# Kernel tuning notes

Hardware: AMD Instinct MI355X
Metric: run time of the kernel (lower is better)

The kernel has to match this reference:

```python
import jax, jax.numpy as jnp
import numpy as np

N_NODES = 100000
N_EDGES = 1600000
IN_CH = 128
HID = 64


def gcn_conv(x, W, b, src, dst, n):
    """PyG-style GCNConv: add self-loops, symmetric deg^-1/2 normalization."""
    h = x @ W  # [n, out]
    # degree including self-loop, computed from destination (col) indices
    deg = jax.ops.segment_sum(jnp.ones_like(dst, dtype=h.dtype), dst, num_segments=n) + 1.0
    dinv = jax.lax.rsqrt(deg)  # [n]
    norm = dinv[src] * dinv[dst]  # [E]
    agg = jax.ops.segment_sum(h[src] * norm[:, None], dst, num_segments=n)
    agg = agg + h * (1.0 / deg)[:, None]  # self-loop term: norm = 1/deg
    return agg + b


def setup_inputs() -> dict:
    key = jax.random.key(0)
    ks = jax.random.split(key, 6)
    x = jax.random.normal(ks[0], (N_NODES, IN_CH), dtype=jnp.float32)
    edge_index = jax.random.randint(ks[1], (2, N_EDGES), 0, N_NODES, dtype=jnp.int64)
    W1 = jax.random.normal(ks[2], (IN_CH, HID), dtype=jnp.float32) / np.sqrt(IN_CH)
    b1 = jnp.zeros((HID,), dtype=jnp.float32)
    W2 = jax.random.normal(ks[3], (HID, HID), dtype=jnp.float32) / np.sqrt(HID)
    b2 = jnp.zeros((HID,), dtype=jnp.float32)
    Wl = jax.random.normal(ks[4], (HID, 1), dtype=jnp.float32) / np.sqrt(HID)
    bl = jnp.zeros((1,), dtype=jnp.float32)
    return {"x": x, "edge_index": edge_index, "W1": W1, "b1": b1,
            "W2": W2, "b2": b2, "Wl": Wl, "bl": bl}


def reference(x, edge_index, W1, b1, W2, b2, Wl, bl):
    src, dst = edge_index[0], edge_index[1]
    n = x.shape[0]
    h = gcn_conv(x, W1, b1, src, dst, n)
    h = jax.nn.relu(h)
    # dropout: identity in eval mode
    h = gcn_conv(h, W2, b2, src, dst, n)
    h = jax.nn.relu(h)
    out = (h @ Wl + bl)[:, 0]  # [n]
    return out
```

## Files before the change

### kernel.cpp

```cpp
#include <hip/hip_runtime.h>
#include <hip/hip_fp16.h>


#define SHIFT 9
#define BSZ   (1 << SHIFT)
#define NBMAX 256
#define BIN_CH 1024
#define PMAX  12288

using f16x8 = __attribute__((ext_vector_type(8))) _Float16;
using f16x2 = __attribute__((ext_vector_type(2))) _Float16;
using f32x4 = __attribute__((ext_vector_type(4))) float;

__global__ __launch_bounds__(256) void k_bin(const int* __restrict__ src,
                                             const int* __restrict__ dst,
                                             unsigned* __restrict__ binned,
                                             int* __restrict__ gbase,
                                             __half* __restrict__ hs,
                                             int n, int nb, int E) {
    if (blockIdx.x == 0 && threadIdx.x < 8) {
        uint4 z = {0u, 0u, 0u, 0u};
        reinterpret_cast<uint4*>(hs + ((size_t)n << 6))[threadIdx.x] = z;
    }
    __shared__ int h[NBMAX];
    __shared__ int ex[NBMAX + 1];
    __shared__ int cur[NBMAX];
    __shared__ int stmp[256];
    const int t = threadIdx.x;
    const int blk = blockIdx.x;
    const int beg = blk * BIN_CH;
    for (int i = t; i < NBMAX; i += 256) h[i] = 0;
    __syncthreads();
    const int e4 = beg + t * 4;
    const bool act = e4 < E;
    int4 d4 = {0, 0, 0, 0};
    if (act) {
        d4 = *reinterpret_cast<const int4*>(dst + e4);
        atomicAdd(&h[d4.x >> SHIFT], 1);
        atomicAdd(&h[d4.y >> SHIFT], 1);
        atomicAdd(&h[d4.z >> SHIFT], 1);
        atomicAdd(&h[d4.w >> SHIFT], 1);
    }
    __syncthreads();
    const int hv = (t < nb) ? h[t] : 0;
    stmp[t] = hv;
    __syncthreads();
    for (int off = 1; off < 256; off <<= 1) {
        int u = (t >= off) ? stmp[t - off] : 0;
        __syncthreads();
        stmp[t] += u;
        __syncthreads();
    }
    if (t <= nb) ex[t] = stmp[t] - ((t < nb) ? h[t] : 0);
    __syncthreads();
    if (t < nb) cur[t] = ex[t];
    if (t <= nb) gbase[(size_t)blk * (nb + 1) + t] = ex[t];
    __syncthreads();
    if (act) {
        const int4 s4 = *reinterpret_cast<const int4*>(src + e4);
        int b0 = d4.x >> SHIFT, b1 = d4.y >> SHIFT;
        int b2 = d4.z >> SHIFT, b3 = d4.w >> SHIFT;
        int p0 = atomicAdd(&cur[b0], 1);
        int p1 = atomicAdd(&cur[b1], 1);
        int p2 = atomicAdd(&cur[b2], 1);
        int p3 = atomicAdd(&cur[b3], 1);
        binned[beg + p0] = (unsigned)s4.x | ((unsigned)(d4.x & (BSZ - 1)) << 17);
        binned[beg + p1] = (unsigned)s4.y | ((unsigned)(d4.y & (BSZ - 1)) << 17);
        binned[beg + p2] = (unsigned)s4.z | ((unsigned)(d4.z & (BSZ - 1)) << 17);
        binned[beg + p3] = (unsigned)s4.w | ((unsigned)(d4.w & (BSZ - 1)) << 17);
    }
}

#define TD 32
__global__ __launch_bounds__(256) void k_xpose(const int* __restrict__ gbase,
                                               int* __restrict__ gbaseT,
                                               int nblk, int nbp1) {
    __shared__ int tile[TD][TD + 1];
    const int ctiles = (nbp1 + TD - 1) / TD;
    const int bx = blockIdx.x % ctiles;
    const int by = blockIdx.x / ctiles;
    const int c0 = bx * TD, r0 = by * TD;
    const int tx = threadIdx.x & 31, ty = threadIdx.x >> 5;
    for (int dy = ty; dy < TD; dy += 8) {
        int r = r0 + dy, c = c0 + tx;
        tile[dy][tx] = (r < nblk && c < nbp1) ? gbase[(size_t)r * nbp1 + c] : 0;
    }
    __syncthreads();
    for (int dy = ty; dy < TD; dy += 8) {
        int r = c0 + dy, c = r0 + tx;
        if (r < nbp1 && c < nblk)
            gbaseT[(size_t)r * nblk + c] = tile[tx][dy];
    }
}

__global__ __launch_bounds__(256) void k_bfill(const unsigned* __restrict__ binned,
                                               const int* __restrict__ gbaseT,
                                               int nblk, int nb,
                                               int* __restrict__ rowptr,
                                               int* __restrict__ colidx,
                                               float* __restrict__ dinv, int n) {
    __shared__ unsigned pedges[PMAX];
    __shared__ int cnt[BSZ];
    __shared__ int nbase[BSZ];
    __shared__ int stmp[256];
    __shared__ int sh_tot;
    const int b = blockIdx.x;
    const int t = threadIdx.x;
    if (t == 0) sh_tot = 0;
    for (int i = t; i < BSZ; i += 256) cnt[i] = 0;
    __syncthreads();
    const int* rowS = gbaseT + (size_t)b * nblk;
    const int* rowE = gbaseT + (size_t)(b + 1) * nblk;
    int ebeg_part = 0;
    for (int blk = t; blk < nblk; blk += 256) {
        const int s0 = rowS[blk];
        const int s1 = rowE[blk];
        ebeg_part += s0;
        const int c = s1 - s0;
        if (c > 0) {
            int pos = atomicAdd(&sh_tot, c);
            const unsigned* bp = binned + (size_t)blk * BIN_CH + s0;
            for (int k = 0; k < c; ++k)
                if (pos + k < PMAX) pedges[pos + k] = bp[k];
        }
    }
    stmp[t] = ebeg_part;
    __syncthreads();
    for (int off = 128; off; off >>= 1) {
        if (t < off) stmp[t] += stmp[t + off];
        __syncthreads();
    }
    const int ebeg = stmp[0];
    const int ecnt = min(sh_tot, PMAX);
    __syncthreads();
    for (int j = t; j < ecnt; j += 256)
        atomicAdd(&cnt[pedges[j] >> 17], 1);
    __syncthreads();
    int c0 = cnt[2 * t], c1 = cnt[2 * t + 1];
    int s = c0 + c1;
    stmp[t] = s;
    __syncthreads();
    for (int off = 1; off < 256; off <<= 1) {
        int u = (t >= off) ? stmp[t - off] : 0;
        __syncthreads();
        stmp[t] += u;
        __syncthreads();
    }
    const int ex = stmp[t] - s;
    nbase[2 * t] = ex;
    nbase[2 * t + 1] = ex + c0;
    __syncthreads();
    const int gb9 = b << SHIFT;
    for (int j = t; j < BSZ; j += 256) {
        const int g = gb9 + j;
        if (g < n) {
            rowptr[g] = (int)(((unsigned)(ebeg + nbase[j]) << 8) |
                              (unsigned)min(cnt[j], 255));
            dinv[g] = rsqrtf((float)cnt[j] + 1.0f);
        }
        cnt[j] = nbase[j];
    }
    __syncthreads();
    for (int j = t; j < ecnt; j += 256) {
        const unsigned e = pedges[j];
        const int lo = (int)(e >> 17);
        const int off = atomicAdd(&cnt[lo], 1);
        colidx[ebeg + off] = (int)((e & 0x1FFFFu) << 7);
    }
}

template <int K, bool A_FP32>
__global__ __launch_bounds__(256) void k_gemm_mfma(const void* __restrict__ Av,
                                                   const float* __restrict__ W,
                                                   const float* __restrict__ dinv,
                                                   __half* __restrict__ C, int n) {
    constexpr int KP = K + 8;
    __shared__ _Float16 Wt[64 * KP];
    const int tid = threadIdx.x;
    for (int i = tid; i < K * 64; i += 256) {
        int k = i >> 6, c = i & 63;
        Wt[c * KP + k] = (_Float16)W[i];
    }
    __syncthreads();

    const int lane = tid & 63;
    const int wv = tid >> 6;
    const int r16 = lane & 15;
    const int kq = lane >> 4;
    const int rb = blockIdx.x * 64 + wv * 16;
    const int arow = min(rb + r16, n - 1);

    f32x4 acc[4] = {{0.f,0.f,0.f,0.f},{0.f,0.f,0.f,0.f},
                    {0.f,0.f,0.f,0.f},{0.f,0.f,0.f,0.f}};

#pragma unroll
    for (int kk = 0; kk < K; kk += 32) {
        f16x8 a;
        if (A_FP32) {
            const float* Ap = (const float*)Av + (size_t)arow * K + kk + kq * 8;
            float4 f0 = *reinterpret_cast<const float4*>(Ap);
            float4 f1 = *reinterpret_cast<const float4*>(Ap + 4);
            a[0] = (_Float16)f0.x; a[1] = (_Float16)f0.y;
            a[2] = (_Float16)f0.z; a[3] = (_Float16)f0.w;
            a[4] = (_Float16)f1.x; a[5] = (_Float16)f1.y;
            a[6] = (_Float16)f1.z; a[7] = (_Float16)f1.w;
        } else {
            const _Float16* Ap = (const _Float16*)Av + (size_t)arow * K + kk + kq * 8;
            a = *reinterpret_cast<const f16x8*>(Ap);
        }
#pragma unroll
        for (int nt = 0; nt < 4; ++nt) {
            f16x8 b = *reinterpret_cast<const f16x8*>(&Wt[(nt * 16 + r16) * KP + kk + kq * 8]);
            acc[nt] = __builtin_amdgcn_mfma_f32_16x16x32_f16(a, b, acc[nt], 0, 0, 0);
        }
    }

#pragma unroll
    for (int r = 0; r < 4; ++r) {
        const int row = rb + kq * 4 + r;
        if (row < n) {
            const float di = dinv[row];
#pragma unroll
            for (int nt = 0; nt < 4; ++nt)
                C[((size_t)row << 6) + nt * 16 + r16] = __float2half(acc[nt][r] * di);
        }
    }
}

__device__ __forceinline__ void dotu4(float acc[8], uint4 u, f16x2 pl, f16x2 ph) {
    union { uint4 u4; f16x2 h[4]; } v;
    v.u4 = u;
    acc[0] = __builtin_amdgcn_fdot2(v.h[0], pl, acc[0], false);
    acc[1] = __builtin_amdgcn_fdot2(v.h[0], ph, acc[1], false);
    acc[2] = __builtin_amdgcn_fdot2(v.h[1], pl, acc[2], false);
    acc[3] = __builtin_amdgcn_fdot2(v.h[1], ph, acc[3], false);
    acc[4] = __builtin_amdgcn_fdot2(v.h[2], pl, acc[4], false);
    acc[5] = __builtin_amdgcn_fdot2(v.h[2], ph, acc[5], false);
    acc[6] = __builtin_amdgcn_fdot2(v.h[3], pl, acc[6], false);
    acc[7] = __builtin_amdgcn_fdot2(v.h[3], ph, acc[7], false);
}

__device__ __forceinline__ void fold8(float acc[8]) {
#pragma unroll
    for (int m = 8; m <= 32; m <<= 1) {
#pragma unroll
        for (int j = 0; j < 8; ++j)
            acc[j] += __shfl_xor(acc[j], m, 64);
    }
}

__device__ __forceinline__ void gather_pair(const char* __restrict__ hsb,
                                            const int* __restrict__ colidx,
                                            unsigned pk0, unsigned pk1,
                                            int g, int p, unsigned dum,
                                            float acc0[8], float acc1[8]) {
    const f16x2 pl = {(_Float16)1.0f, (_Float16)0.0f};
    const f16x2 ph = {(_Float16)0.0f, (_Float16)1.0f};
    const int beg0 = (int)(pk0 >> 8), deg0 = (int)(pk0 & 255u);
    const int beg1 = (int)(pk1 >> 8), deg1 = (int)(pk1 & 255u);
    const int t0 = deg0 - g, t1 = deg1 - g;
    const unsigned poff = (unsigned)(p << 4);
    const unsigned dumo = dum + poff;
    const int ia = beg0 + g;
    const int ib = beg1 + g;
    unsigned a0 = (unsigned)colidx[ia]      + poff;
    unsigned a1 = (unsigned)colidx[ia + 8]  + poff;
    unsigned a2 = (unsigned)colidx[ia + 16] + poff;
    unsigned a3 = (unsigned)colidx[ia + 24] + poff;
    unsigned b0 = (unsigned)colidx[ib]      + poff;
    unsigned b1 = (unsigned)colidx[ib + 8]  + poff;
    unsigned b2 = (unsigned)colidx[ib + 16] + poff;
    unsigned b3 = (unsigned)colidx[ib + 24] + poff;
    unsigned oa0 = (0  < t0) ? a0 : dumo;
    unsigned oa1 = (8  < t0) ? a1 : dumo;
    unsigned oa2 = (16 < t0) ? a2 : dumo;
    unsigned oa3 = (24 < t0) ? a3 : dumo;
    unsigned ob0 = (0  < t1) ? b0 : dumo;
    unsigned ob1 = (8  < t1) ? b1 : dumo;
    unsigned ob2 = (16 < t1) ? b2 : dumo;
    unsigned ob3 = (24 < t1) ? b3 : dumo;
    uint4 ua0 = *reinterpret_cast<const uint4*>(hsb + oa0);
    uint4 ua1 = *reinterpret_cast<const uint4*>(hsb + oa1);
    uint4 ua2 = *reinterpret_cast<const uint4*>(hsb + oa2);
    uint4 ua3 = *reinterpret_cast<const uint4*>(hsb + oa3);
    uint4 ub0 = *reinterpret_cast<const uint4*>(hsb + ob0);
    uint4 ub1 = *reinterpret_cast<const uint4*>(hsb + ob1);
    uint4 ub2 = *reinterpret_cast<const uint4*>(hsb + ob2);
    uint4 ub3 = *reinterpret_cast<const uint4*>(hsb + ob3);
    dotu4(acc0, ua0, pl, ph);
    dotu4(acc0, ua1, pl, ph);
    dotu4(acc0, ua2, pl, ph);
    dotu4(acc0, ua3, pl, ph);
    dotu4(acc1, ub0, pl, ph);
    dotu4(acc1, ub1, pl, ph);
    dotu4(acc1, ub2, pl, ph);
    dotu4(acc1, ub3, pl, ph);
    const int ns0 = (deg0 + 7) >> 3;
    for (int k = 4; k < ns0; k += 4) {
        const int ik = beg0 + 8 * k + g;
        unsigned c0 = (unsigned)colidx[ik]      + poff;
        unsigned c1 = (unsigned)colidx[ik + 8]  + poff;
        unsigned c2 = (unsigned)colidx[ik + 16] + poff;
        unsigned c3 = (unsigned)colidx[ik + 24] + poff;
        const int kb = 8 * k;
        uint4 u0 = *reinterpret_cast<const uint4*>(hsb + ((kb      < t0) ? c0 : dumo));
        uint4 u1 = *reinterpret_cast<const uint4*>(hsb + ((kb + 8  < t0) ? c1 : dumo));
        uint4 u2 = *reinterpret_cast<const uint4*>(hsb + ((kb + 16 < t0) ? c2 : dumo));
        uint4 u3 = *reinterpret_cast<const uint4*>(hsb + ((kb + 24 < t0) ? c3 : dumo));
        dotu4(acc0, u0, pl, ph);
        dotu4(acc0, u1, pl, ph);
        dotu4(acc0, u2, pl, ph);
        dotu4(acc0, u3, pl, ph);
    }
    const int ns1 = (deg1 + 7) >> 3;
    for (int k = 4; k < ns1; k += 4) {
        const int ik = beg1 + 8 * k + g;
        unsigned c0 = (unsigned)colidx[ik]      + poff;
        unsigned c1 = (unsigned)colidx[ik + 8]  + poff;
        unsigned c2 = (unsigned)colidx[ik + 16] + poff;
        unsigned c3 = (unsigned)colidx[ik + 24] + poff;
        const int kb = 8 * k;
        uint4 u0 = *reinterpret_cast<const uint4*>(hsb + ((kb      < t1) ? c0 : dumo));
        uint4 u1 = *reinterpret_cast<const uint4*>(hsb + ((kb + 8  < t1) ? c1 : dumo));
        uint4 u2 = *reinterpret_cast<const uint4*>(hsb + ((kb + 16 < t1) ? c2 : dumo));
        uint4 u3 = *reinterpret_cast<const uint4*>(hsb + ((kb + 24 < t1) ? c3 : dumo));
        dotu4(acc1, u0, pl, ph);
        dotu4(acc1, u1, pl, ph);
        dotu4(acc1, u2, pl, ph);
        dotu4(acc1, u3, pl, ph);
    }
    fold8(acc0);
    fold8(acc1);
}

__global__ __launch_bounds__(256) void k_agg_relu(const __half* __restrict__ hs,
                                                  const int* __restrict__ rowptr,
                                                  const int* __restrict__ colidx,
                                                  const float* __restrict__ dinv,
                                                  const float* __restrict__ b,
                                                  __half* __restrict__ out, int n) {
    const int wv = threadIdx.x >> 6;
    const int i0 = blockIdx.x * 8 + wv * 2;
    const int lane = threadIdx.x & 63;
    if (i0 >= n) return;
    const int i1 = min(i0 + 1, n - 1);
    const int g = lane >> 3, p = lane & 7;
    const int iw = (lane & 8) ? i1 : i0;
    const unsigned pk0 = (unsigned)rowptr[i0];
    const unsigned pk1 = (unsigned)rowptr[i1];
    uint4 su = *reinterpret_cast<const uint4*>(hs + ((size_t)iw << 6) + (p << 3));
    const float di = dinv[iw];
    float acc0[8] = {}, acc1[8] = {};
    gather_pair((const char*)hs, colidx, pk0, pk1, g, p, (unsigned)n << 7,
                acc0, acc1);
    if (lane < 16) {
        const f16x2 pl = {(_Float16)1.0f, (_Float16)0.0f};
        const f16x2 ph = {(_Float16)0.0f, (_Float16)1.0f};
        float a[8];
#pragma unroll
        for (int j = 0; j < 8; ++j) a[j] = (lane & 8) ? acc1[j] : acc0[j];
        dotu4(a, su, pl, ph);
        float4 b0 = *reinterpret_cast<const float4*>(b + (p << 3));
        float4 b1 = *reinterpret_cast<const float4*>(b + (p << 3) + 4);
        __half2 h0 = __halves2half2(__float2half(fmaxf(fmaf(a[0], di, b0.x), 0.f)),
                                    __float2half(fmaxf(fmaf(a[1], di, b0.y), 0.f)));
        __half2 h1 = __halves2half2(__float2half(fmaxf(fmaf(a[2], di, b0.z), 0.f)),
                                    __float2half(fmaxf(fmaf(a[3], di, b0.w), 0.f)));
        __half2 h2 = __halves2half2(__float2half(fmaxf(fmaf(a[4], di, b1.x), 0.f)),
                                    __float2half(fmaxf(fmaf(a[5], di, b1.y), 0.f)));
        __half2 h3 = __halves2half2(__float2half(fmaxf(fmaf(a[6], di, b1.z), 0.f)),
                                    __float2half(fmaxf(fmaf(a[7], di, b1.w), 0.f)));
        uint4 u;
        u.x = *reinterpret_cast<unsigned*>(&h0);
        u.y = *reinterpret_cast<unsigned*>(&h1);
        u.z = *reinterpret_cast<unsigned*>(&h2);
        u.w = *reinterpret_cast<unsigned*>(&h3);
        if (iw < n && (i0 + 1 < n || !(lane & 8)))
            *reinterpret_cast<uint4*>(out + ((size_t)iw << 6) + (p << 3)) = u;
    }
}

__global__ __launch_bounds__(256) void k_agg_head(const __half* __restrict__ hs,
                                                  const int* __restrict__ rowptr,
                                                  const int* __restrict__ colidx,
                                                  const float* __restrict__ dinv,
                                                  const float* __restrict__ b2,
                                                  const float* __restrict__ Wl,
                                                  const float* __restrict__ bl,
                                                  float* __restrict__ out, int n) {
    const int wv = threadIdx.x >> 6;
    const int i0 = blockIdx.x * 8 + wv * 2;
    const int lane = threadIdx.x & 63;
    if (i0 >= n) return;
    const int i1 = min(i0 + 1, n - 1);
    const int g = lane >> 3, p = lane & 7;
    const int iw = (lane & 8) ? i1 : i0;
    const unsigned pk0 = (unsigned)rowptr[i0];
    const unsigned pk1 = (unsigned)rowptr[i1];
    uint4 su = *reinterpret_cast<const uint4*>(hs + ((size_t)iw << 6) + (p << 3));
    const float di = dinv[iw];
    float acc0[8] = {}, acc1[8] = {};
    gather_pair((const char*)hs, colidx, pk0, pk1, g, p, (unsigned)n << 7,
                acc0, acc1);
    const f16x2 pl = {(_Float16)1.0f, (_Float16)0.0f};
    const f16x2 ph = {(_Float16)0.0f, (_Float16)1.0f};
    float a[8];
#pragma unroll
    for (int j = 0; j < 8; ++j) a[j] = (lane & 8) ? acc1[j] : acc0[j];
    dotu4(a, su, pl, ph);
    float4 b0 = *reinterpret_cast<const float4*>(b2 + (p << 3));
    float4 b1 = *reinterpret_cast<const float4*>(b2 + (p << 3) + 4);
    float4 w0 = *reinterpret_cast<const float4*>(Wl + (p << 3));
    float4 w1 = *reinterpret_cast<const float4*>(Wl + (p << 3) + 4);
    float v = fmaxf(fmaf(a[0], di, b0.x), 0.f) * w0.x
            + fmaxf(fmaf(a[1], di, b0.y), 0.f) * w0.y
            + fmaxf(fmaf(a[2], di, b0.z), 0.f) * w0.z
            + fmaxf(fmaf(a[3], di, b0.w), 0.f) * w0.w
            + fmaxf(fmaf(a[4], di, b1.x), 0.f) * w1.x
            + fmaxf(fmaf(a[5], di, b1.y), 0.f) * w1.y
            + fmaxf(fmaf(a[6], di, b1.z), 0.f) * w1.z
            + fmaxf(fmaf(a[7], di, b1.w), 0.f) * w1.w;
    v += __shfl_xor(v, 1, 64);
    v += __shfl_xor(v, 2, 64);
    v += __shfl_xor(v, 4, 64);
    if (lane == 0) out[i0] = v + bl[0];
    if (lane == 8 && i0 + 1 < n) out[i1] = v + bl[0];
}

extern "C" void kernel_launch(void* const* d_in, const int* in_sizes, int n_in,
                              void* d_out, int out_size, void* d_ws, size_t ws_size,
                              hipStream_t stream) {
    const float* x  = (const float*)d_in[0];
    const int*   ei = (const int*)d_in[1];
    const float* W1 = (const float*)d_in[2];
    const float* b1 = (const float*)d_in[3];
    const float* W2 = (const float*)d_in[4];
    const float* b2 = (const float*)d_in[5];
    const float* Wl = (const float*)d_in[6];
    const float* bl = (const float*)d_in[7];
    float* out = (float*)d_out;

    const int n = in_sizes[0] / 128;
    const int E = in_sizes[1] / 2;
    const int* src = ei;
    const int* dst = ei + E;
    const int nb = (n + BSZ - 1) >> SHIFT;
    const int nblk = (E + BIN_CH - 1) / BIN_CH;

    char* ws = (char*)d_ws;
    size_t o = 0;
    auto alloc = [&](size_t bytes) {
        void* p = ws + o;
        o = (o + bytes + 255) & ~(size_t)255;
        return p;
    };
    float* dinv    = (float*)alloc((size_t)n * 4);
    int*   rowptr  = (int*)  alloc((size_t)(n + 1) * 4);
    int*   colidx  = (int*)  alloc(((size_t)E + 64) * 4);
    int*   gbase   = (int*)  alloc((size_t)nblk * (nb + 1) * 4);
    int*   gbaseT  = (int*)  alloc((size_t)(nb + 1) * nblk * 4);
    __half* hs     = (__half*)alloc((size_t)(n + 1) * 64 * 2);
    __half* bufA   = (__half*)alloc((size_t)n * 64 * 2);
    unsigned* binned = (unsigned*)alloc(((size_t)nblk * BIN_CH) * 4);

    k_bin<<<nblk, 256, 0, stream>>>(src, dst, binned, gbase, hs, n, nb, E);
    const int ctiles = (nb + 1 + TD - 1) / TD;
    const int rtiles = (nblk + TD - 1) / TD;
    k_xpose<<<ctiles * rtiles, 256, 0, stream>>>(gbase, gbaseT, nblk, nb + 1);
    k_bfill<<<nb, 256, 0, stream>>>(binned, gbaseT, nblk, nb, rowptr, colidx,
                                    dinv, n);

    k_gemm_mfma<128, true><<<(n + 63) / 64, 256, 0, stream>>>(x, W1, dinv, hs, n);
    k_agg_relu<<<(n + 7) / 8, 256, 0, stream>>>(hs, rowptr, colidx, dinv, b1, bufA, n);

    k_gemm_mfma<64, false><<<(n + 63) / 64, 256, 0, stream>>>(bufA, W2, dinv, hs, n);
    k_agg_head<<<(n + 7) / 8, 256, 0, stream>>>(hs, rowptr, colidx, dinv, b2, Wl, bl,
                                                out, n);
}
```

Baseline: 157.7 us.

## Widen bucket-fill kernel to 1024 threads with scan-based edge placement

```diff
diff --git a/kernel.cpp b/kernel.cpp
--- a/kernel.cpp
+++ b/kernel.cpp
@@ -6,7 +6,7 @@
 #define BSZ   (1 << SHIFT)
 #define NBMAX 256
 #define BIN_CH 1024
-#define PMAX  12288
+#define PMAX  11776
 
 using f16x8 = __attribute__((ext_vector_type(8))) _Float16;
 using f16x2 = __attribute__((ext_vector_type(2))) _Float16;
@@ -93,65 +93,87 @@
     }
 }
 
-__global__ __launch_bounds__(256) void k_bfill(const unsigned* __restrict__ binned,
-                                               const int* __restrict__ gbaseT,
-                                               int nblk, int nb,
-                                               int* __restrict__ rowptr,
-                                               int* __restrict__ colidx,
-                                               float* __restrict__ dinv, int n) {
+__global__ __launch_bounds__(1024) void k_bfill(const unsigned* __restrict__ binned,
+                                                const int* __restrict__ gbaseT,
+                                                int nblk, int nb,
+                                                int* __restrict__ rowptr,
+                                                int* __restrict__ colidx,
+                                                float* __restrict__ dinv, int n) {
     __shared__ unsigned pedges[PMAX];
+    __shared__ int segarr[2048];
+    __shared__ int stmp[1024];
     __shared__ int cnt[BSZ];
     __shared__ int nbase[BSZ];
-    __shared__ int stmp[256];
-    __shared__ int sh_tot;
     const int b = blockIdx.x;
     const int t = threadIdx.x;
-    if (t == 0) sh_tot = 0;
-    for (int i = t; i < BSZ; i += 256) cnt[i] = 0;
-    __syncthreads();
     const int* rowS = gbaseT + (size_t)b * nblk;
     const int* rowE = gbaseT + (size_t)(b + 1) * nblk;
-    int ebeg_part = 0;
-    for (int blk = t; blk < nblk; blk += 256) {
+    for (int i = t; i < BSZ; i += 1024) cnt[i] = 0;
+    int eb = 0;
+    {
+        int l0 = 0, l1 = 0;
+        if (t < nblk)        { int s0 = rowS[t];        l0 = rowE[t] - s0;        eb += s0; }
+        if (t + 1024 < nblk) { int s0 = rowS[t + 1024]; l1 = rowE[t + 1024] - s0; eb += s0; }
+        segarr[t] = l0;
+        segarr[t + 1024] = l1;
+    }
+    stmp[t] = eb;
+    __syncthreads();
+    for (int off = 512; off; off >>= 1) {
+        if (t < off) stmp[t] += stmp[t + off];
+        __syncthreads();
+    }
+    const int ebeg = stmp[0];
+    __syncthreads();
+    const int a0 = segarr[2 * t];
+    const int a1 = segarr[2 * t + 1];
+    const int ps = a0 + a1;
+    stmp[t] = ps;
+    __syncthreads();
+    for (int off = 1; off < 1024; off <<= 1) {
+        int u = (t >= off) ? stmp[t - off] : 0;
+        __syncthreads();
+        stmp[t] += u;
+        __syncthreads();
+    }
+    const int ecnt = min(stmp[1023], PMAX);
+    const int exp2_ = stmp[t] - ps;
+    segarr[2 * t] = exp2_;
+    segarr[2 * t + 1] = exp2_ + a0;
+    __syncthreads();
+    for (int blk = t; blk < nblk; blk += 1024) {
         const int s0 = rowS[blk];
-        const int s1 = rowE[blk];
-        ebeg_part += s0;
-        const int c = s1 - s0;
-        if (c > 0) {
-            int pos = atomicAdd(&sh_tot, c);
-            const unsigned* bp = binned + (size_t)blk * BIN_CH + s0;
-            for (int k = 0; k < c; ++k)
-                if (pos + k < PMAX) pedges[pos + k] = bp[k];
+        const int c = rowE[blk] - s0;
+        const int pos = segarr[blk];
+        const unsigned* bp = binned + (size_t)blk * BIN_CH + s0;
+        for (int k = 0; k < c; ++k) {
+            const int d = pos + k;
+            if (d < PMAX) pedges[d] = bp[k];
         }
     }
-    stmp[t] = ebeg_part;
-    __syncthreads();
-    for (int off = 128; off; off >>= 1) {
-        if (t < off) stmp[t] += stmp[t + off];
-        __syncthreads();
-    }
-    const int ebeg = stmp[0];
-    const int ecnt = min(sh_tot, PMAX);
-    __syncthreads();
-    for (int j = t; j < ecnt; j += 256)
+    __syncthreads();
+    for (int j = t; j < ecnt; j += 1024)
         atomicAdd(&cnt[pedges[j] >> 17], 1);
     __syncthreads();
-    int c0 = cnt[2 * t], c1 = cnt[2 * t + 1];
-    int s = c0 + c1;
-    stmp[t] = s;
+    const int c0 = (t < 256) ? cnt[2 * t] : 0;
+    const int c1 = (t < 256) ? cnt[2 * t + 1] : 0;
+    const int s2 = c0 + c1;
+    stmp[t] = s2;
     __syncthreads();
     for (int off = 1; off < 256; off <<= 1) {
-        int u = (t >= off) ? stmp[t - off] : 0;
-        __syncthreads();
-        stmp[t] += u;
-        __syncthreads();
-    }
-    const int ex = stmp[t] - s;
-    nbase[2 * t] = ex;
-    nbase[2 * t + 1] = ex + c0;
+        int u = (t >= off && t < 256) ? stmp[t - off] : 0;
+        __syncthreads();
+        if (t < 256) stmp[t] += u;
+        __syncthreads();
+    }
+    if (t < 256) {
+        const int ex = stmp[t] - s2;
+        nbase[2 * t] = ex;
+        nbase[2 * t + 1] = ex + c0;
+    }
     __syncthreads();
     const int gb9 = b << SHIFT;
-    for (int j = t; j < BSZ; j += 256) {
+    for (int j = t; j < BSZ; j += 1024) {
         const int g = gb9 + j;
         if (g < n) {
             rowptr[g] = (int)(((unsigned)(ebeg + nbase[j]) << 8) |
@@ -161,7 +183,7 @@
         cnt[j] = nbase[j];
     }
     __syncthreads();
-    for (int j = t; j < ecnt; j += 256) {
+    for (int j = t; j < ecnt; j += 1024) {
         const unsigned e = pedges[j];
         const int lo = (int)(e >> 17);
         const int off = atomicAdd(&cnt[lo], 1);
@@ -467,8 +489,8 @@
     const int ctiles = (nb + 1 + TD - 1) / TD;
     const int rtiles = (nblk + TD - 1) / TD;
     k_xpose<<<ctiles * rtiles, 256, 0, stream>>>(gbase, gbaseT, nblk, nb + 1);
-    k_bfill<<<nb, 256, 0, stream>>>(binned, gbaseT, nblk, nb, rowptr, colidx,
-                                    dinv, n);
+    k_bfill<<<nb, 1024, 0, stream>>>(binned, gbaseT, nblk, nb, rowptr, colidx,
+                                     dinv, n);
 
     k_gemm_mfma<128, true><<<(n + 63) / 64, 256, 0, stream>>>(x, W1, dinv, hs, n);
     k_agg_relu<<<(n + 7) / 8, 256, 0, stream>>>(hs, rowptr, colidx, dinv, b1, bufA, n);
```

Result: faster. 133.1 us (median of 2 runs) (-15.6%).
